# Performance work log

Measured on AMD Instinct MI355X. Metric: run time of the kernel, lower is better.

The kernel has to match this reference:

```python
import jax, jax.numpy as jnp
import numpy as np

B, DZ, M_, N_ = 2048, 256, 64, 64
GAMMA, EPS, MAXITERS = 1.0, 1e-6, 1000


def sinkhorn(Mcost):
    # entropic OT with uniform marginals r=1/m, c=1/n (ddn sinkhorn, non-logspace)
    b, h, w = Mcost.shape
    r = 1.0 / h
    c = 1.0 / w
    P = jnp.exp(-GAMMA * Mcost)
    P = P / jnp.sum(P, axis=(1, 2), keepdims=True)

    def cond_fn(state):
        P, it, err = state
        return jnp.logical_and(it < MAXITERS, err > EPS)

    def body_fn(state):
        P, it, _ = state
        alpha = jnp.sum(P, axis=2, keepdims=True)   # row sums (B,h,1)
        P = P * (r / alpha)                          # row normalize to r
        beta = jnp.sum(P, axis=1, keepdims=True)    # col sums (B,1,w)
        err = jnp.max(jnp.abs(beta - c))
        # torch loop breaks BEFORE col-normalizing when converged
        P = jnp.where(err <= EPS, P, P * (c / beta))
        return P, it + 1, err

    init_err = jnp.array(jnp.inf, dtype=Mcost.dtype)
    P, _, _ = jax.lax.while_loop(cond_fn, body_fn, (P, jnp.array(0, jnp.int32), init_err))
    return P


def setup_inputs() -> dict:
    key = jax.random.key(0)
    ks = jax.random.split(key, 7)
    H = M_ * N_
    z = jax.random.normal(ks[0], (B, DZ), dtype=jnp.float32)
    W1 = jax.random.normal(ks[1], (DZ, H), dtype=jnp.float32) * (1.0 / np.sqrt(DZ))
    b1 = jnp.zeros((H,), jnp.float32)
    W2 = jax.random.normal(ks[2], (H, H), dtype=jnp.float32) * (1.0 / np.sqrt(H))
    b2 = jnp.zeros((H,), jnp.float32)
    W3 = jax.random.normal(ks[3], (H, H), dtype=jnp.float32) * (1.0 / np.sqrt(H))
    b3 = jnp.zeros((H,), jnp.float32)
    return {"z": z, "W1": W1, "b1": b1, "W2": W2, "b2": b2, "W3": W3, "b3": b3}


def reference(z, W1, b1, W2, b2, W3, b3):
    x = jax.nn.relu(z @ W1 + b1)
    x = jax.nn.relu(x @ W2 + b2)
    x = x @ W3 + b3
    x = x.reshape(z.shape[0], M_, N_)  # (B, m, n) cost matrix
    return sinkhorn(x)
```

## Files before the change

kernel.cpp:

```cpp
#include <hip/hip_runtime.h>
#include <hip/hip_bf16.h>

typedef unsigned short ushort_t;
typedef __attribute__((ext_vector_type(8))) short bf16x8;
typedef __attribute__((ext_vector_type(4))) float f32x4;

#define MDIM 2048
#define NDIM 4096

__device__ __forceinline__ ushort_t to_bf16(float f) {
    __hip_bfloat16 h = __float2bfloat16(f);
    return *reinterpret_cast<ushort_t*>(&h);
}

__global__ void cast_bf16_kernel(const float* __restrict__ in, ushort_t* __restrict__ out, int n) {
    int i = blockIdx.x * blockDim.x + threadIdx.x;
    if (i < n) out[i] = to_bf16(in[i]);
}

__global__ void transpose_cast_kernel(const float* __restrict__ W, ushort_t* __restrict__ WT,
                                      int K, int N) {
    __shared__ float tile[32][33];
    const int tx = threadIdx.x, ty = threadIdx.y;
    const int n0 = blockIdx.x * 32, k0 = blockIdx.y * 32;
#pragma unroll
    for (int r = 0; r < 4; ++r)
        tile[ty + r * 8][tx] = W[(size_t)(k0 + ty + r * 8) * N + n0 + tx];
    __syncthreads();
    const int t = ty * 32 + tx;
    const int nl = t >> 3;
    const int kc = (t & 7) * 4;
    ushort4 o;
    o.x = to_bf16(tile[kc + 0][nl]);
    o.y = to_bf16(tile[kc + 1][nl]);
    o.z = to_bf16(tile[kc + 2][nl]);
    o.w = to_bf16(tile[kc + 3][nl]);
    *reinterpret_cast<ushort4*>(&WT[(size_t)(n0 + nl) * K + k0 + kc]) = o;
}

template <typename OutT, bool RELU>
__global__ __launch_bounds__(256, 2) void gemm_bt(const ushort_t* __restrict__ A,
                                                  const ushort_t* __restrict__ BT,
                                                  const float* __restrict__ bias,
                                                  OutT* __restrict__ C, int Kdim) {
    __shared__ __align__(16) ushort_t As[128 * 40];
    __shared__ __align__(16) ushort_t Bs[128 * 40];

    const int t = threadIdx.x;
    const int m0 = blockIdx.y * 128;
    const int n0 = blockIdx.x * 128;
    const int lane = t & 63;
    const int wid = t >> 6;
    const int quad = lane >> 4;
    const int l16 = lane & 15;
    const int wm = (wid & 1) * 64;
    const int wn = (wid >> 1) * 64;

    f32x4 acc[4][4];
#pragma unroll
    for (int i = 0; i < 4; ++i)
#pragma unroll
        for (int j = 0; j < 4; ++j) acc[i][j] = (f32x4){0.f, 0.f, 0.f, 0.f};

    const int row_a = t >> 2;
    const int cc = t & 3;

    const ushort_t* pA0 = A + (size_t)(m0 + row_a) * Kdim + cc * 8;
    const ushort_t* pA1 = A + (size_t)(m0 + row_a + 64) * Kdim + cc * 8;
    const ushort_t* pB0 = BT + (size_t)(n0 + row_a) * Kdim + cc * 8;
    const ushort_t* pB1 = BT + (size_t)(n0 + row_a + 64) * Kdim + cc * 8;

    uint4 av0 = *reinterpret_cast<const uint4*>(pA0);
    uint4 av1 = *reinterpret_cast<const uint4*>(pA1);
    uint4 bv0 = *reinterpret_cast<const uint4*>(pB0);
    uint4 bv1 = *reinterpret_cast<const uint4*>(pB1);

    for (int k0 = 0; k0 < Kdim; k0 += 32) {
        __syncthreads();
        *reinterpret_cast<uint4*>(&As[row_a * 40 + cc * 8]) = av0;
        *reinterpret_cast<uint4*>(&As[(row_a + 64) * 40 + cc * 8]) = av1;
        *reinterpret_cast<uint4*>(&Bs[row_a * 40 + cc * 8]) = bv0;
        *reinterpret_cast<uint4*>(&Bs[(row_a + 64) * 40 + cc * 8]) = bv1;
        __syncthreads();

        if (k0 + 32 < Kdim) {
            av0 = *reinterpret_cast<const uint4*>(pA0 + k0 + 32);
            av1 = *reinterpret_cast<const uint4*>(pA1 + k0 + 32);
            bv0 = *reinterpret_cast<const uint4*>(pB0 + k0 + 32);
            bv1 = *reinterpret_cast<const uint4*>(pB1 + k0 + 32);
        }

        bf16x8 af[4], bfr[4];
#pragma unroll
        for (int i = 0; i < 4; ++i)
            af[i] = *reinterpret_cast<const bf16x8*>(&As[(wm + i * 16 + l16) * 40 + quad * 8]);
#pragma unroll
        for (int j = 0; j < 4; ++j)
            bfr[j] = *reinterpret_cast<const bf16x8*>(&Bs[(wn + j * 16 + l16) * 40 + quad * 8]);
#pragma unroll
        for (int i = 0; i < 4; ++i)
#pragma unroll
            for (int j = 0; j < 4; ++j)
                acc[i][j] = __builtin_amdgcn_mfma_f32_16x16x32_bf16(af[i], bfr[j], acc[i][j], 0, 0, 0);
    }

#pragma unroll
    for (int i = 0; i < 4; ++i) {
#pragma unroll
        for (int r = 0; r < 4; ++r) {
            const int grow = m0 + wm + i * 16 + quad * 4 + r;
#pragma unroll
            for (int j = 0; j < 4; ++j) {
                const int gcol = n0 + wn + j * 16 + l16;
                float v = acc[i][j][r] + bias[gcol];
                if (RELU) v = fmaxf(v, 0.0f);
                if constexpr (sizeof(OutT) == 2) {
                    C[(size_t)grow * NDIM + gcol] = to_bf16(v);
                } else {
                    C[(size_t)grow * NDIM + gcol] = v;
                }
            }
        }
    }
}

__device__ __forceinline__ float rdl(float v, int l) {
    return __uint_as_float(__builtin_amdgcn_readlane(__float_as_uint(v), l));
}

__global__ __launch_bounds__(64) void sinkhorn_kernel(float* __restrict__ PM) {
    __shared__ __align__(16) float T[64 * 65];
    const int l = threadIdx.x;
    float* base = PM + (size_t)blockIdx.x * 4096;

    float Kcol[64];
    float Krow[64];
#pragma unroll
    for (int r = 0; r < 64; ++r)
        Kcol[r] = __expf(-base[r * 64 + l]);
#pragma unroll
    for (int r = 0; r < 64; ++r)
        T[r * 65 + l] = Kcol[r];
    __syncthreads();
#pragma unroll
    for (int c = 0; c < 64; ++c)
        Krow[c] = T[l * 65 + c];

    float a = 0.0f, b = 1.0f;
    for (int it = 0; it < 1000; ++it) {
        float t1 = 0.0f;
#pragma unroll
        for (int c = 0; c < 64; ++c)
            t1 = fmaf(Krow[c], rdl(b, c), t1);
        a = 0.015625f / t1;

        float t2 = 0.0f;
#pragma unroll
        for (int r = 0; r < 64; ++r)
            t2 = fmaf(Kcol[r], rdl(a, r), t2);
        const float err = fabsf(b * t2 - 0.015625f);
        if (__ballot(err > 1e-6f) == 0ull) break;
        b = 0.015625f / t2;
    }

#pragma unroll
    for (int r = 0; r < 64; ++r)
        base[r * 64 + l] = rdl(a, r) * Kcol[r] * b;
}

extern "C" void kernel_launch(void* const* d_in, const int* in_sizes, int n_in,
                              void* d_out, int out_size, void* d_ws, size_t ws_size,
                              hipStream_t stream) {
    const float* z  = (const float*)d_in[0];
    const float* W1 = (const float*)d_in[1];
    const float* b1 = (const float*)d_in[2];
    const float* W2 = (const float*)d_in[3];
    const float* b2 = (const float*)d_in[4];
    const float* W3 = (const float*)d_in[5];
    const float* b3 = (const float*)d_in[6];
    float* out = (float*)d_out;
    char* ws = (char*)d_ws;

    ushort_t* W2T = (ushort_t*)(ws + 0);
    ushort_t* W3T = (ushort_t*)(ws + (size_t)33554432);
    ushort_t* C1b = (ushort_t*)(ws + (size_t)67108864);
    ushort_t* C2b = (ushort_t*)(ws + (size_t)83886080);
    ushort_t* Zb  = (ushort_t*)(ws + (size_t)100663296);
    ushort_t* W1T = (ushort_t*)(ws + (size_t)101711872);

    cast_bf16_kernel<<<2048, 256, 0, stream>>>(z, Zb, MDIM * 256);
    transpose_cast_kernel<<<dim3(128, 8), dim3(32, 8), 0, stream>>>(W1, W1T, 256, 4096);
    transpose_cast_kernel<<<dim3(128, 128), dim3(32, 8), 0, stream>>>(W2, W2T, 4096, 4096);
    transpose_cast_kernel<<<dim3(128, 128), dim3(32, 8), 0, stream>>>(W3, W3T, 4096, 4096);

    gemm_bt<ushort_t, true><<<dim3(NDIM / 128, MDIM / 128), 256, 0, stream>>>(Zb, W1T, b1, C1b, 256);
    gemm_bt<ushort_t, true><<<dim3(NDIM / 128, MDIM / 128), 256, 0, stream>>>(C1b, W2T, b2, C2b, 4096);
    gemm_bt<float, false><<<dim3(NDIM / 128, MDIM / 128), 256, 0, stream>>>(C2b, W3T, b3, out, 4096);

    sinkhorn_kernel<<<2048, 64, 0, stream>>>(out);
}
```

Measured before the change: 384.9 us.

## Rewrite GEMM with triple-buffered direct-to-LDS loads and larger 128x256 tiles

The GEMM now uses 512-thread blocks computing 128x256 tiles with K-step 64. Tiles are staged straight from global memory into LDS through global_load_lds, triple-buffered with XOR-swizzled layout. The global loads for the next tile are interleaved with MFMA phases under s_setprio and explicit barriers and waitcnts. This is meant to hide memory latency and cut LDS bank conflicts and register staging, in exchange for more LDS use (~144KB per block, which may limit occupancy) and fragile hand-written synchronization.

```diff
diff --git a/kernel.cpp b/kernel.cpp
--- a/kernel.cpp
+++ b/kernel.cpp
@@ -38,23 +38,30 @@
     *reinterpret_cast<ushort4*>(&WT[(size_t)(n0 + nl) * K + k0 + kc]) = o;
 }
 
+
+#define GLD(gp, lp) __builtin_amdgcn_global_load_lds(                      \
+        (const __attribute__((address_space(1))) void*)(gp),               \
+        (__attribute__((address_space(3))) void*)(lp), 16, 0, 0)
+
+#define MFMA(d, a, b) d = __builtin_amdgcn_mfma_f32_16x16x32_bf16(a, b, d, 0, 0, 0)
+
 template <typename OutT, bool RELU>
-__global__ __launch_bounds__(256, 2) void gemm_bt(const ushort_t* __restrict__ A,
+__global__ __launch_bounds__(512, 2) void gemm_p8(const ushort_t* __restrict__ A,
                                                   const ushort_t* __restrict__ BT,
                                                   const float* __restrict__ bias,
                                                   OutT* __restrict__ C, int Kdim) {
-    __shared__ __align__(16) ushort_t As[128 * 40];
-    __shared__ __align__(16) ushort_t Bs[128 * 40];
+    __shared__ __align__(16) ushort_t As[3][128 * 64];
+    __shared__ __align__(16) ushort_t Bs[3][256 * 64];
 
     const int t = threadIdx.x;
+    const int l = t & 63;
+    const int w = t >> 6;
+    const int l16 = l & 15;
+    const int quad = l >> 4;
+    const int wr = w >> 2;
+    const int wc = w & 3;
     const int m0 = blockIdx.y * 128;
-    const int n0 = blockIdx.x * 128;
-    const int lane = t & 63;
-    const int wid = t >> 6;
-    const int quad = lane >> 4;
-    const int l16 = lane & 15;
-    const int wm = (wid & 1) * 64;
-    const int wn = (wid >> 1) * 64;
+    const int n0 = blockIdx.x * 256;
 
     f32x4 acc[4][4];
 #pragma unroll
@@ -62,56 +69,108 @@
 #pragma unroll
         for (int j = 0; j < 4; ++j) acc[i][j] = (f32x4){0.f, 0.f, 0.f, 0.f};
 
-    const int row_a = t >> 2;
-    const int cc = t & 3;
-
-    const ushort_t* pA0 = A + (size_t)(m0 + row_a) * Kdim + cc * 8;
-    const ushort_t* pA1 = A + (size_t)(m0 + row_a + 64) * Kdim + cc * 8;
-    const ushort_t* pB0 = BT + (size_t)(n0 + row_a) * Kdim + cc * 8;
-    const ushort_t* pB1 = BT + (size_t)(n0 + row_a + 64) * Kdim + cc * 8;
-
-    uint4 av0 = *reinterpret_cast<const uint4*>(pA0);
-    uint4 av1 = *reinterpret_cast<const uint4*>(pA1);
-    uint4 bv0 = *reinterpret_cast<const uint4*>(pB0);
-    uint4 bv1 = *reinterpret_cast<const uint4*>(pB1);
-
-    for (int k0 = 0; k0 < Kdim; k0 += 32) {
-        __syncthreads();
-        *reinterpret_cast<uint4*>(&As[row_a * 40 + cc * 8]) = av0;
-        *reinterpret_cast<uint4*>(&As[(row_a + 64) * 40 + cc * 8]) = av1;
-        *reinterpret_cast<uint4*>(&Bs[row_a * 40 + cc * 8]) = bv0;
-        *reinterpret_cast<uint4*>(&Bs[(row_a + 64) * 40 + cc * 8]) = bv1;
-        __syncthreads();
-
-        if (k0 + 32 < Kdim) {
-            av0 = *reinterpret_cast<const uint4*>(pA0 + k0 + 32);
-            av1 = *reinterpret_cast<const uint4*>(pA1 + k0 + 32);
-            bv0 = *reinterpret_cast<const uint4*>(pB0 + k0 + 32);
-            bv1 = *reinterpret_cast<const uint4*>(pB1 + k0 + 32);
-        }
-
-        bf16x8 af[4], bfr[4];
-#pragma unroll
-        for (int i = 0; i < 4; ++i)
-            af[i] = *reinterpret_cast<const bf16x8*>(&As[(wm + i * 16 + l16) * 40 + quad * 8]);
-#pragma unroll
-        for (int j = 0; j < 4; ++j)
-            bfr[j] = *reinterpret_cast<const bf16x8*>(&Bs[(wn + j * 16 + l16) * 40 + quad * 8]);
-#pragma unroll
-        for (int i = 0; i < 4; ++i)
-#pragma unroll
-            for (int j = 0; j < 4; ++j)
-                acc[i][j] = __builtin_amdgcn_mfma_f32_16x16x32_bf16(af[i], bfr[j], acc[i][j], 0, 0, 0);
+    const int srow = w * 8 + (l >> 3);
+    const int scol = ((l & 7) ^ (l >> 3)) * 8;
+    const ushort_t* gA0 = A  + (size_t)(m0 + srow) * Kdim + scol;
+    const ushort_t* gA1 = A  + (size_t)(m0 + 64 + srow) * Kdim + scol;
+    const ushort_t* gB0 = BT + (size_t)(n0 + srow) * Kdim + scol;
+    const ushort_t* gB1 = BT + (size_t)(n0 + 64 + srow) * Kdim + scol;
+    const ushort_t* gB2 = BT + (size_t)(n0 + 128 + srow) * Kdim + scol;
+    const ushort_t* gB3 = BT + (size_t)(n0 + 192 + srow) * Kdim + scol;
+    const int ldsW = w * 8 * 64;
+
+    const int swz = l16 & 7;
+#define LDA_(buf, i, kk) (*(const bf16x8*)&As[buf][(wr * 64 + (i) * 16 + l16) * 64 + ((((kk) * 4 + quad) ^ swz) * 8)])
+#define LDB_(buf, j, kk) (*(const bf16x8*)&Bs[buf][(wc * 64 + (j) * 16 + l16) * 64 + ((((kk) * 4 + quad) ^ swz) * 8)])
+
+#define STAGE_TILE(buf, koff) do {                      \
+        GLD(gA0 + (koff), &As[buf][ldsW]);              \
+        GLD(gA1 + (koff), &As[buf][ldsW + 64 * 64]);    \
+        GLD(gB0 + (koff), &Bs[buf][ldsW]);              \
+        GLD(gB1 + (koff), &Bs[buf][ldsW + 64 * 64]);    \
+        GLD(gB2 + (koff), &Bs[buf][ldsW + 128 * 64]);   \
+        GLD(gB3 + (koff), &Bs[buf][ldsW + 192 * 64]);   \
+    } while (0)
+
+#define PHASE_BEGIN()                                       \
+        __builtin_amdgcn_s_barrier();                       \
+        asm volatile("s_waitcnt lgkmcnt(0)" ::: "memory");  \
+        __builtin_amdgcn_s_setprio(1)
+#define PHASE_END()                                         \
+        __builtin_amdgcn_s_setprio(0);                      \
+        __builtin_amdgcn_s_barrier()
+
+#define MFMA8(r0, r1, A0, A1)                                      \
+        MFMA(acc[r0][0], A0, b0); MFMA(acc[r0][1], A0, b1);        \
+        MFMA(acc[r0][2], A0, b2); MFMA(acc[r0][3], A0, b3);        \
+        MFMA(acc[r1][0], A1, b0); MFMA(acc[r1][1], A1, b1);        \
+        MFMA(acc[r1][2], A1, b2); MFMA(acc[r1][3], A1, b3)
+
+    const int nt = Kdim >> 6;
+
+    STAGE_TILE(0, 0);
+    STAGE_TILE(1, 64);
+    asm volatile("s_waitcnt vmcnt(6)" ::: "memory");
+    __builtin_amdgcn_s_barrier();
+
+    for (int tt = 0; tt < nt; ++tt) {
+        const int buf = tt % 3;
+        const int nb = (tt + 2) % 3;
+        const int koff = (tt + 2) << 6;
+        const bool more = (tt + 2) < nt;
+
+        bf16x8 a0, a1, b0, b1, b2, b3;
+
+        a0 = LDA_(buf, 0, 0); a1 = LDA_(buf, 1, 0);
+        b0 = LDB_(buf, 0, 0); b1 = LDB_(buf, 1, 0);
+        b2 = LDB_(buf, 2, 0); b3 = LDB_(buf, 3, 0);
+        if (more) {
+            GLD(gA0 + koff, &As[nb][ldsW]);
+            GLD(gA1 + koff, &As[nb][ldsW + 64 * 64]);
+        }
+        PHASE_BEGIN();
+        MFMA8(0, 1, a0, a1);
+        PHASE_END();
+
+        a0 = LDA_(buf, 2, 0); a1 = LDA_(buf, 3, 0);
+        if (more) {
+            GLD(gB0 + koff, &Bs[nb][ldsW]);
+            GLD(gB1 + koff, &Bs[nb][ldsW + 64 * 64]);
+        }
+        PHASE_BEGIN();
+        MFMA8(2, 3, a0, a1);
+        PHASE_END();
+
+        a0 = LDA_(buf, 0, 1); a1 = LDA_(buf, 1, 1);
+        b0 = LDB_(buf, 0, 1); b1 = LDB_(buf, 1, 1);
+        b2 = LDB_(buf, 2, 1); b3 = LDB_(buf, 3, 1);
+        if (more) {
+            GLD(gB2 + koff, &Bs[nb][ldsW + 128 * 64]);
+            GLD(gB3 + koff, &Bs[nb][ldsW + 192 * 64]);
+        }
+        PHASE_BEGIN();
+        MFMA8(0, 1, a0, a1);
+        PHASE_END();
+
+        a0 = LDA_(buf, 2, 1); a1 = LDA_(buf, 3, 1);
+        PHASE_BEGIN();
+        MFMA8(2, 3, a0, a1);
+        __builtin_amdgcn_s_setprio(0);
+        if (tt + 1 < nt) {
+            if (more) asm volatile("s_waitcnt vmcnt(6)" ::: "memory");
+            else      asm volatile("s_waitcnt vmcnt(0)" ::: "memory");
+        }
+        __builtin_amdgcn_s_barrier();
     }
 
 #pragma unroll
     for (int i = 0; i < 4; ++i) {
 #pragma unroll
         for (int r = 0; r < 4; ++r) {
-            const int grow = m0 + wm + i * 16 + quad * 4 + r;
+            const int grow = m0 + wr * 64 + i * 16 + quad * 4 + r;
 #pragma unroll
             for (int j = 0; j < 4; ++j) {
-                const int gcol = n0 + wn + j * 16 + l16;
+                const int gcol = n0 + wc * 64 + j * 16 + l16;
                 float v = acc[i][j][r] + bias[gcol];
                 if (RELU) v = fmaxf(v, 0.0f);
                 if constexpr (sizeof(OutT) == 2) {
@@ -193,9 +252,9 @@
     transpose_cast_kernel<<<dim3(128, 128), dim3(32, 8), 0, stream>>>(W2, W2T, 4096, 4096);
     transpose_cast_kernel<<<dim3(128, 128), dim3(32, 8), 0, stream>>>(W3, W3T, 4096, 4096);
 
-    gemm_bt<ushort_t, true><<<dim3(NDIM / 128, MDIM / 128), 256, 0, stream>>>(Zb, W1T, b1, C1b, 256);
-    gemm_bt<ushort_t, true><<<dim3(NDIM / 128, MDIM / 128), 256, 0, stream>>>(C1b, W2T, b2, C2b, 4096);
-    gemm_bt<float, false><<<dim3(NDIM / 128, MDIM / 128), 256, 0, stream>>>(C2b, W3T, b3, out, 4096);
+    gemm_p8<ushort_t, true><<<dim3(NDIM / 256, MDIM / 128), 512, 0, stream>>>(Zb, W1T, b1, C1b, 256);
+    gemm_p8<ushort_t, true><<<dim3(NDIM / 256, MDIM / 128), 512, 0, stream>>>(C1b, W2T, b2, C2b, 4096);
+    gemm_p8<float, false><<<dim3(NDIM / 256, MDIM / 128), 512, 0, stream>>>(C2b, W3T, b3, out, 4096);
 
     sinkhorn_kernel<<<2048, 64, 0, stream>>>(out);
 }
```

Result: slower. 394.2 us (+2.4%).
